# Performance work log

Measured on AMD Instinct MI355X. Metric: run time of the kernel, lower is better.

The kernel has to match this reference:

```python
import jax, jax.numpy as jnp
import numpy as np
import math

B, T, D, H = 4, 2048, 1024, 16
DK = D // H  # 64


def setup_inputs() -> dict:
    key = jax.random.key(0)
    ks = jax.random.split(key, 9)
    s = 0.02
    return {
        "x": jax.random.normal(ks[0], (B, T, D), jnp.float32),
        "wq": jax.random.normal(ks[1], (H, DK, D), jnp.float32) * s,
        "bq": jax.random.normal(ks[2], (H, DK), jnp.float32) * s,
        "wk": jax.random.normal(ks[3], (H, DK, D), jnp.float32) * s,
        "bk": jax.random.normal(ks[4], (H, DK), jnp.float32) * s,
        "wv": jax.random.normal(ks[5], (H, DK, D), jnp.float32) * s,
        "bv": jax.random.normal(ks[6], (H, DK), jnp.float32) * s,
        "wo": jax.random.normal(ks[7], (D, D), jnp.float32) * s,
        "bo": jax.random.normal(ks[8], (D,), jnp.float32) * s,
    }


def reference(x, wq, bq, wk, bk, wv, bv, wo, bo):
    # per-head projections (torch Linear: y = x @ W.T + b), all heads batched
    q = jnp.einsum("btc,hdc->bhtd", x, wq) + bq[None, :, None, :]
    k = jnp.einsum("btc,hdc->bhtd", x, wk) + bk[None, :, None, :]
    v = jnp.einsum("btc,hdc->bhtd", x, wv) + bv[None, :, None, :]
    scores = jnp.einsum("bhtd,bhsd->bhts", q, k) / math.sqrt(DK)
    causal = jnp.tril(jnp.ones((T, T), dtype=bool))  # True = keep
    scores = jnp.where(causal[None, None], scores, -jnp.inf)
    sm = jax.nn.softmax(scores, axis=-1)
    att = jnp.einsum("bhts,bhsd->bhtd", sm, v)
    # concat heads (head 0 first) -> [B, T, D]
    yh = att.transpose(0, 2, 1, 3).reshape(B, T, D)
    return yh @ wo.T + bo
```

## Files before the change

kernel.cpp:

```cpp
#include <hip/hip_runtime.h>
#include <hip/hip_bf16.h>
#include <cstdint>
#include <cstddef>

#define B_  4
#define T_  2048
#define D_  1024
#define H_  16
#define DK_ 64
#define M_  (B_ * T_)
#define NT8 (D_ / 64)

typedef __attribute__((ext_vector_type(8))) short bf16x8;
typedef __attribute__((ext_vector_type(4))) float f32x4;

static __device__ __forceinline__ unsigned short f2bf(float f) {
    __hip_bfloat16 h = __float2bfloat16(f);
    unsigned short u;
    __builtin_memcpy(&u, &h, 2);
    return u;
}

static __device__ __forceinline__ unsigned int pk2bf(float a, float b) {
    __hip_bfloat162 h = __float22bfloat162_rn(make_float2(a, b));
    unsigned int u;
    __builtin_memcpy(&u, &h, 4);
    return u;
}

static __device__ __forceinline__ void gl2lds16(const void* g, void* l) {
    __builtin_amdgcn_global_load_lds(
        (const __attribute__((address_space(1))) unsigned int*)g,
        (__attribute__((address_space(3))) unsigned int*)l,
        16, 0, 0);
}

__global__ __launch_bounds__(256) void cvt_bf16(
    const float* __restrict__ x,  const float* __restrict__ wq,
    const float* __restrict__ wk, const float* __restrict__ wv,
    const float* __restrict__ wo, unsigned short* __restrict__ dst)
{
    const int idx = blockIdx.x * 256 + threadIdx.x;
    const float* src;
    int off;
    if (idx < 2097152) { src = x; off = idx; }
    else {
        const int r = (idx - 2097152) >> 18;
        off = (idx - 2097152) & 262143;
        src = (r == 0) ? wq : (r == 1) ? wk : (r == 2) ? wv : wo;
    }
    float4 v = ((const float4*)src)[off];
    ushort4 o;
    o.x = f2bf(v.x); o.y = f2bf(v.y); o.z = f2bf(v.z); o.w = f2bf(v.w);
    ((ushort4*)dst)[idx] = o;
}

__global__ __launch_bounds__(512, 2) void gemm8p(
    const unsigned short* __restrict__ Amat,
    const unsigned short* __restrict__ w0,
    const unsigned short* __restrict__ w1,
    const unsigned short* __restrict__ w2,
    const float* __restrict__ b0,
    const float* __restrict__ b1,
    const float* __restrict__ b2,
    unsigned short* __restrict__ outU,
    float* __restrict__ outF,
    const int mode)
{
    const int s   = blockIdx.x;
    const int xcd = s & 7;
    const int idx = s >> 3;
    const int mm  = idx & 3;
    const int ns  = idx >> 2;
    const int sel = (mode == 0) ? (ns >> 3) : 3;
    const int nn  = (mode == 0) ? (ns & 7) : ns;
    const int m0  = (xcd * 4 + mm) * 256;
    const int n0  = nn * 128;

    const unsigned short* Bmat = (sel == 0) ? w0 : (sel == 1) ? w1 : w2;
    const float* bias          = (sel == 0) ? b0 : (sel == 1) ? b1 : b2;
    const bool selV = (sel == 2);

    const int tid  = threadIdx.x;
    const int w    = tid >> 6;
    const int lane = tid & 63;
    const int l15  = lane & 15, g = lane >> 4;
    const int lane8 = lane * 8;
    const int wm8  = (w >> 2) * 8;
    const int wn2  = (w & 3) * 2;

    __shared__ __align__(16) unsigned short As[2][32][512];
    __shared__ __align__(16) unsigned short Bs[2][16][512];

    f32x4 acc[8][2];
#pragma unroll
    for (int i = 0; i < 8; ++i)
#pragma unroll
        for (int j = 0; j < 2; ++j) acc[i][j] = (f32x4){0.f, 0.f, 0.f, 0.f};

    const unsigned short* aP[4];
#pragma unroll
    for (int j = 0; j < 4; ++j)
        aP[j] = Amat + (size_t)(m0 + (w >> 1) * 16 + 64 * j + l15) * D_
                     + (w & 1) * 32 + g * 8;
    const unsigned short* bP[2];
#pragma unroll
    for (int jb = 0; jb < 2; ++jb)
        bP[jb] = Bmat + (size_t)(n0 + w * 16 + l15) * D_ + jb * 32 + g * 8;

#pragma unroll
    for (int j = 0; j < 4; ++j) gl2lds16(aP[j], &As[0][w + 8 * j][0]);
    gl2lds16(bP[0], &Bs[0][2 * w    ][0]);
    gl2lds16(bP[1], &Bs[0][2 * w + 1][0]);
    gl2lds16(aP[0] + 64, &As[1][w     ][0]);
    gl2lds16(aP[2] + 64, &As[1][w + 16][0]);
    gl2lds16(bP[0] + 64, &Bs[1][2 * w    ][0]);
    gl2lds16(bP[1] + 64, &Bs[1][2 * w + 1][0]);
    asm volatile("s_waitcnt vmcnt(4)" ::: "memory");
    __builtin_amdgcn_s_barrier();

    bf16x8 bfr[2][2];
    bf16x8 ap[4][2];

    for (int kt = 0; kt < NT8; ++kt) {
        const int cur = kt & 1;
        const int ko  = kt * 64;

#pragma unroll
        for (int nj = 0; nj < 2; ++nj)
#pragma unroll
            for (int ks = 0; ks < 2; ++ks)
                bfr[nj][ks] = *(const bf16x8*)&Bs[cur][(wn2 + nj) * 2 + ks][lane8];
#pragma unroll
        for (int mi = 0; mi < 4; ++mi)
#pragma unroll
            for (int ks = 0; ks < 2; ++ks)
                ap[mi][ks] = *(const bf16x8*)&As[cur][(wm8 + mi) * 2 + ks][lane8];
        if (kt + 1 < NT8) {
            gl2lds16(aP[1] + ko + 64, &As[cur ^ 1][w + 8 ][0]);
            gl2lds16(aP[3] + ko + 64, &As[cur ^ 1][w + 24][0]);
        }
        __builtin_amdgcn_s_barrier();
        asm volatile("s_waitcnt lgkmcnt(0)" ::: "memory");
        __builtin_amdgcn_s_setprio(1);
        if (!selV) {
#pragma unroll
            for (int mi = 0; mi < 4; ++mi)
#pragma unroll
                for (int nj = 0; nj < 2; ++nj) {
                    acc[mi][nj] = __builtin_amdgcn_mfma_f32_16x16x32_bf16(
                        bfr[nj][0], ap[mi][0], acc[mi][nj], 0, 0, 0);
                    acc[mi][nj] = __builtin_amdgcn_mfma_f32_16x16x32_bf16(
                        bfr[nj][1], ap[mi][1], acc[mi][nj], 0, 0, 0);
                }
        } else {
#pragma unroll
            for (int mi = 0; mi < 4; ++mi)
#pragma unroll
                for (int nj = 0; nj < 2; ++nj) {
                    acc[mi][nj] = __builtin_amdgcn_mfma_f32_16x16x32_bf16(
                        ap[mi][0], bfr[nj][0], acc[mi][nj], 0, 0, 0);
                    acc[mi][nj] = __builtin_amdgcn_mfma_f32_16x16x32_bf16(
                        ap[mi][1], bfr[nj][1], acc[mi][nj], 0, 0, 0);
                }
        }
        __builtin_amdgcn_s_setprio(0);
        __builtin_amdgcn_s_barrier();

#pragma unroll
        for (int mi = 0; mi < 4; ++mi)
#pragma unroll
            for (int ks = 0; ks < 2; ++ks)
                ap[mi][ks] = *(const bf16x8*)&As[cur][(wm8 + 4 + mi) * 2 + ks][lane8];
        if (kt + 2 < NT8) {
            gl2lds16(aP[0] + ko + 128, &As[cur][w     ][0]);
            gl2lds16(aP[2] + ko + 128, &As[cur][w + 16][0]);
            gl2lds16(bP[0] + ko + 128, &Bs[cur][2 * w    ][0]);
            gl2lds16(bP[1] + ko + 128, &Bs[cur][2 * w + 1][0]);
        }
        __builtin_amdgcn_s_barrier();
        asm volatile("s_waitcnt lgkmcnt(0)" ::: "memory");
        __builtin_amdgcn_s_setprio(1);
        if (!selV) {
#pragma unroll
            for (int mi = 0; mi < 4; ++mi)
#pragma unroll
                for (int nj = 0; nj < 2; ++nj) {
                    acc[4 + mi][nj] = __builtin_amdgcn_mfma_f32_16x16x32_bf16(
                        bfr[nj][0], ap[mi][0], acc[4 + mi][nj], 0, 0, 0);
                    acc[4 + mi][nj] = __builtin_amdgcn_mfma_f32_16x16x32_bf16(
                        bfr[nj][1], ap[mi][1], acc[4 + mi][nj], 0, 0, 0);
                }
        } else {
#pragma unroll
            for (int mi = 0; mi < 4; ++mi)
#pragma unroll
                for (int nj = 0; nj < 2; ++nj) {
                    acc[4 + mi][nj] = __builtin_amdgcn_mfma_f32_16x16x32_bf16(
                        ap[mi][0], bfr[nj][0], acc[4 + mi][nj], 0, 0, 0);
                    acc[4 + mi][nj] = __builtin_amdgcn_mfma_f32_16x16x32_bf16(
                        ap[mi][1], bfr[nj][1], acc[4 + mi][nj], 0, 0, 0);
                }
        }
        __builtin_amdgcn_s_setprio(0);
        if (kt < NT8 - 2)       asm volatile("s_waitcnt vmcnt(4)" ::: "memory");
        else if (kt == NT8 - 2) asm volatile("s_waitcnt vmcnt(0)" ::: "memory");
        __builtin_amdgcn_s_barrier();
    }

    const int mbase = m0 + (w >> 2) * 128;
    const int nbase = n0 + (w & 3) * 32;
    const size_t BTD = (size_t)B_ * T_ * D_;

    if (mode == 1) {
#pragma unroll
        for (int nj = 0; nj < 2; ++nj) {
            const int ch0 = nbase + nj * 16 + g * 4;
            const float4 bb = *(const float4*)(bias + ch0);
#pragma unroll
            for (int mi = 0; mi < 8; ++mi) {
                const int tok = mbase + mi * 16 + l15;
                float4 r;
                r.x = acc[mi][nj][0] + bb.x;
                r.y = acc[mi][nj][1] + bb.y;
                r.z = acc[mi][nj][2] + bb.z;
                r.w = acc[mi][nj][3] + bb.w;
                *(float4*)(outF + (size_t)tok * D_ + ch0) = r;
            }
        }
    } else if (!selV) {
        unsigned short* outp = outU + (size_t)sel * BTD;
        const float osc = (sel == 0) ? 0.125f * 1.44269504f : 1.0f;
#pragma unroll
        for (int nj = 0; nj < 2; ++nj) {
            const int ch0 = nbase + nj * 16 + g * 4;
            const int hh = ch0 >> 6, dk0 = ch0 & 63;
            const float4 bb = *(const float4*)(bias + ch0);
#pragma unroll
            for (int mi = 0; mi < 8; ++mi) {
                const int tok = mbase + mi * 16 + l15;
                const int b = tok >> 11, t = tok & (T_ - 1);
                ushort4 r;
                r.x = f2bf((acc[mi][nj][0] + bb.x) * osc);
                r.y = f2bf((acc[mi][nj][1] + bb.y) * osc);
                r.z = f2bf((acc[mi][nj][2] + bb.z) * osc);
                r.w = f2bf((acc[mi][nj][3] + bb.w) * osc);
                *(ushort4*)(outp + ((size_t)((b * H_ + hh) * T_ + t)) * DK_ + dk0) = r;
            }
        }
    } else {
        unsigned short* outp = outU + 2 * BTD;
#pragma unroll
        for (int nj = 0; nj < 2; ++nj) {
            const int ch = nbase + nj * 16 + l15;
            const int hh = ch >> 6, dk = ch & 63;
            const float bbv = bias[ch];
#pragma unroll
            for (int mi = 0; mi < 8; ++mi) {
                const int tok0 = mbase + mi * 16 + g * 4;
                const int b = tok0 >> 11, t0 = tok0 & (T_ - 1);
                ushort4 r;
                r.x = f2bf(acc[mi][nj][0] + bbv);
                r.y = f2bf(acc[mi][nj][1] + bbv);
                r.z = f2bf(acc[mi][nj][2] + bbv);
                r.w = f2bf(acc[mi][nj][3] + bbv);
                *(ushort4*)(outp + ((size_t)((b * H_ + hh) * DK_ + dk)) * T_ + t0) = r;
            }
        }
    }
}

__global__ __launch_bounds__(256) void attn(
    const unsigned short* __restrict__ qg, const unsigned short* __restrict__ kg,
    const unsigned short* __restrict__ vtg,
    float* __restrict__ pO, float* __restrict__ pL,
    unsigned short* __restrict__ yh)
{
    const int s    = blockIdx.x;
    const int xcd  = s & 7;
    const int t_   = s >> 3;
    const int bhl  = t_ / 48;
    const int j    = t_ % 48;
    const int bh   = xcd * 8 + bhl;
    const int ridx = 47 - j;

    int x, ks;
    if (ridx < 16) { x = ridx; ks = 0; }
    else { const int r = ridx - 16; x = 16 + (r >> 1); ks = r & 1; }
    const int h   = bh & (H_ - 1);
    const int b   = bh >> 4;
    const int tq0 = x * 64;
    const int sBeg = ks << 10;
    const int sEnd = min(sBeg + 1024, tq0 + 64);
    const int nCh  = (sEnd - sBeg) >> 6;

    const int tid  = threadIdx.x;
    const int w    = tid >> 6;
    const int lane = tid & 63;
    const int l15  = lane & 15;
    const int g    = lane >> 4;

    const size_t base = (size_t)bh * T_ * DK_;
    const unsigned short* Qb  = qg  + base;
    const unsigned short* Kb  = kg  + base;
    const unsigned short* Vtb = vtg + base;

    __shared__ __align__(16) unsigned short Kf[8][512];
    __shared__ __align__(16) unsigned short Vf[8][512];
    __shared__ __align__(16) unsigned short Pb[4][16][68];

    const int q0w = tq0 + w * 16;
    const int tq  = q0w + l15;

    bf16x8 qf0 = *(const bf16x8*)(Qb + (size_t)tq * DK_ + g * 8);
    bf16x8 qf1 = *(const bf16x8*)(Qb + (size_t)tq * DK_ + 32 + g * 8);

    bf16x8 ones;
#pragma unroll
    for (int jj = 0; jj < 8; ++jj) ones[jj] = (short)0x3F80;

    f32x4 o[4];
#pragma unroll
    for (int i = 0; i < 4; ++i) o[i] = (f32x4){0.f, 0.f, 0.f, 0.f};
    f32x4 lacc = {0.f, 0.f, 0.f, 0.f};

    const unsigned short* kSrc = Kb + (size_t)(sBeg + w * 16 + l15) * DK_ + g * 8;
    const unsigned short* vSrc = Vtb + (size_t)(w * 16 + l15) * T_ + sBeg + g * 8;

    bf16x8 kr0 = *(const bf16x8*)(kSrc);
    bf16x8 kr1 = *(const bf16x8*)(kSrc + 32);
    bf16x8 vr0 = *(const bf16x8*)(vSrc);
    bf16x8 vr1 = *(const bf16x8*)(vSrc + 32);

    for (int ch = 0; ch < nCh; ++ch) {
        const int s0 = sBeg + ch * 64;
        __syncthreads();
        *(bf16x8*)&Kf[2 * w    ][lane * 8] = kr0;
        *(bf16x8*)&Kf[2 * w + 1][lane * 8] = kr1;
        *(bf16x8*)&Vf[2 * w    ][lane * 8] = vr0;
        *(bf16x8*)&Vf[2 * w + 1][lane * 8] = vr1;
        if (ch + 1 < nCh) {
            const size_t ko = (size_t)(ch + 1) * 64 * DK_;
            const int    vo = (ch + 1) * 64;
            kr0 = *(const bf16x8*)(kSrc + ko);
            kr1 = *(const bf16x8*)(kSrc + ko + 32);
            vr0 = *(const bf16x8*)(vSrc + vo);
            vr1 = *(const bf16x8*)(vSrc + vo + 32);
        }
        __syncthreads();

#pragma unroll
        for (int st = 0; st < 4; ++st) {
            const int sbase = s0 + st * 16;
            const bool live = (sbase <= q0w + 15);
            unsigned int pkl, pkh;
            if (live) {
                bf16x8 a0 = *(const bf16x8*)&Kf[st * 2 + 0][lane * 8];
                bf16x8 a1 = *(const bf16x8*)&Kf[st * 2 + 1][lane * 8];
                f32x4 sacc = {0.f, 0.f, 0.f, 0.f};
                sacc = __builtin_amdgcn_mfma_f32_16x16x32_bf16(a0, qf0, sacc, 0, 0, 0);
                sacc = __builtin_amdgcn_mfma_f32_16x16x32_bf16(a1, qf1, sacc, 0, 0, 0);
                float p0, p1, p2, p3;
                if (sbase + 15 > q0w) {
                    p0 = (sbase + g * 4 + 0 <= tq) ? exp2f(sacc[0]) : 0.f;
                    p1 = (sbase + g * 4 + 1 <= tq) ? exp2f(sacc[1]) : 0.f;
                    p2 = (sbase + g * 4 + 2 <= tq) ? exp2f(sacc[2]) : 0.f;
                    p3 = (sbase + g * 4 + 3 <= tq) ? exp2f(sacc[3]) : 0.f;
                } else {
                    p0 = exp2f(sacc[0]); p1 = exp2f(sacc[1]);
                    p2 = exp2f(sacc[2]); p3 = exp2f(sacc[3]);
                }
                pkl = pk2bf(p0, p1);
                pkh = pk2bf(p2, p3);
            } else {
                pkl = 0; pkh = 0;
            }
            uint2 pk; pk.x = pkl; pk.y = pkh;
            *(uint2*)&Pb[w][l15][st * 16 + g * 4] = pk;
        }

        bf16x8 pf0 = *(const bf16x8*)&Pb[w][l15][g * 8];
        bf16x8 pf1 = *(const bf16x8*)&Pb[w][l15][32 + g * 8];
        lacc = __builtin_amdgcn_mfma_f32_16x16x32_bf16(ones, pf0, lacc, 0, 0, 0);
        lacc = __builtin_amdgcn_mfma_f32_16x16x32_bf16(ones, pf1, lacc, 0, 0, 0);
#pragma unroll
        for (int dt = 0; dt < 4; ++dt) {
            bf16x8 v0 = *(const bf16x8*)&Vf[dt * 2 + 0][lane * 8];
            bf16x8 v1 = *(const bf16x8*)&Vf[dt * 2 + 1][lane * 8];
            o[dt] = __builtin_amdgcn_mfma_f32_16x16x32_bf16(v0, pf0, o[dt], 0, 0, 0);
            o[dt] = __builtin_amdgcn_mfma_f32_16x16x32_bf16(v1, pf1, o[dt], 0, 0, 0);
        }
    }

    if (tq0 < 1024) {
        const float inv = 1.f / lacc[0];
        unsigned short* yrow = yh + ((size_t)(b * T_ + tq)) * D_ + h * DK_;
#pragma unroll
        for (int dt = 0; dt < 4; ++dt) {
            ushort4 r;
            r.x = f2bf(o[dt][0] * inv); r.y = f2bf(o[dt][1] * inv);
            r.z = f2bf(o[dt][2] * inv); r.w = f2bf(o[dt][3] * inv);
            *(ushort4*)(yrow + dt * 16 + g * 4) = r;
        }
    } else {
        float* po = pO + ((size_t)ks * (B_ * H_) + bh) * (size_t)T_ * DK_
                       + (size_t)tq * DK_;
#pragma unroll
        for (int dt = 0; dt < 4; ++dt) {
            float4 r;
            r.x = o[dt][0]; r.y = o[dt][1]; r.z = o[dt][2]; r.w = o[dt][3];
            *(float4*)(po + dt * 16 + g * 4) = r;
        }
        if (g == 0)
            pL[((size_t)ks * (B_ * H_) + bh) * T_ + tq] = lacc[0];
    }
}

__global__ __launch_bounds__(256) void attn_reduce(
    const float* __restrict__ pO, const float* __restrict__ pL,
    unsigned short* __restrict__ yh)
{
    const int idx  = blockIdx.x * 256 + threadIdx.x;
    const int flat = idx * 4;
    const int dk = flat & 63;
    const int t  = 1024 + ((flat >> 6) & 1023);
    const int bh = flat >> 16;
    const int h = bh & (H_ - 1), b = bh >> 4;

    const size_t e0 = ((size_t)bh * T_ + t) * DK_ + dk;
    const size_t soff = (size_t)(B_ * H_) * T_ * DK_;
    float4 o  = *(const float4*)(pO + e0);
    float4 o1 = *(const float4*)(pO + soff + e0);
    o.x += o1.x; o.y += o1.y; o.z += o1.z; o.w += o1.w;
    const float l = pL[(size_t)bh * T_ + t]
                  + pL[(size_t)(B_ * H_) * T_ + (size_t)bh * T_ + t];
    const float inv = 1.f / l;
    ushort4 r;
    r.x = f2bf(o.x * inv); r.y = f2bf(o.y * inv);
    r.z = f2bf(o.z * inv); r.w = f2bf(o.w * inv);
    *(ushort4*)(yh + ((size_t)(b * T_ + t)) * D_ + h * DK_ + dk) = r;
}

extern "C" void kernel_launch(void* const* d_in, const int* in_sizes, int n_in,
                              void* d_out, int out_size, void* d_ws, size_t ws_size,
                              hipStream_t stream) {
    const float* x  = (const float*)d_in[0];
    const float* wq = (const float*)d_in[1];
    const float* bq = (const float*)d_in[2];
    const float* wk = (const float*)d_in[3];
    const float* bk = (const float*)d_in[4];
    const float* wv = (const float*)d_in[5];
    const float* bv = (const float*)d_in[6];
    const float* wo = (const float*)d_in[7];
    const float* bo = (const float*)d_in[8];
    float* out = (float*)d_out;

    const size_t BTD = (size_t)B_ * T_ * D_;
    const size_t WSZ = (size_t)D_ * D_;
    unsigned short* xb  = (unsigned short*)d_ws;
    unsigned short* wqb = xb  + BTD;
    unsigned short* wkb = wqb + WSZ;
    unsigned short* wvb = wkb + WSZ;
    unsigned short* wob = wvb + WSZ;
    unsigned short* qb  = wob + WSZ;
    unsigned short* kb  = qb  + BTD;
    unsigned short* vtb = kb  + BTD;
    unsigned short* yhb = vtb + BTD;
    float* pO = (float*)(yhb + BTD);
    float* pL = pO + 2 * BTD;

    cvt_bf16<<<dim3(12288), 256, 0, stream>>>(x, wq, wk, wv, wo, xb);

    gemm8p<<<dim3(768), 512, 0, stream>>>(
        xb, wqb, wkb, wvb, bq, bk, bv, qb, (float*)nullptr, 0);

    attn<<<dim3(3072), 256, 0, stream>>>(qb, kb, vtb, pO, pL, yhb);

    attn_reduce<<<dim3(4096), 256, 0, stream>>>(pO, pL, yhb);

    gemm8p<<<dim3(256), 512, 0, stream>>>(
        yhb, wob, wob, wob, bo, bo, bo, (unsigned short*)nullptr, out, 1);
}
```

Before: 328.7 us.

## Double attention query tile to 128 rows per block, two 16-row groups per wave

Each attention block now processes 128 query rows instead of 64, with each wave handling two 16-row query sub-tiles that share the same K/V fragments loaded from shared memory. This halves the block count and the K/V global and LDS loads per query row, and wave chunks entirely above the causal diagonal are now skipped. The cost is more registers per thread (two accumulator sets), larger P staging in shared memory, and fewer blocks, which may reduce occupancy and load balance.

```diff
diff --git a/kernel.cpp b/kernel.cpp
--- a/kernel.cpp
+++ b/kernel.cpp
@@ -279,19 +279,19 @@
     const int s    = blockIdx.x;
     const int xcd  = s & 7;
     const int t_   = s >> 3;
-    const int bhl  = t_ / 48;
-    const int j    = t_ % 48;
+    const int bhl  = t_ / 24;
+    const int j    = t_ % 24;
     const int bh   = xcd * 8 + bhl;
-    const int ridx = 47 - j;
+    const int ridx = 23 - j;
 
     int x, ks;
-    if (ridx < 16) { x = ridx; ks = 0; }
-    else { const int r = ridx - 16; x = 16 + (r >> 1); ks = r & 1; }
+    if (ridx < 8) { x = ridx; ks = 0; }
+    else { const int r = ridx - 8; x = 8 + (r >> 1); ks = r & 1; }
     const int h   = bh & (H_ - 1);
     const int b   = bh >> 4;
-    const int tq0 = x * 64;
+    const int tq0 = x * 128;
     const int sBeg = ks << 10;
-    const int sEnd = min(sBeg + 1024, tq0 + 64);
+    const int sEnd = min(sBeg + 1024, tq0 + 128);
     const int nCh  = (sEnd - sBeg) >> 6;
 
     const int tid  = threadIdx.x;
@@ -307,22 +307,29 @@
 
     __shared__ __align__(16) unsigned short Kf[8][512];
     __shared__ __align__(16) unsigned short Vf[8][512];
-    __shared__ __align__(16) unsigned short Pb[4][16][68];
-
-    const int q0w = tq0 + w * 16;
-    const int tq  = q0w + l15;
-
-    bf16x8 qf0 = *(const bf16x8*)(Qb + (size_t)tq * DK_ + g * 8);
-    bf16x8 qf1 = *(const bf16x8*)(Qb + (size_t)tq * DK_ + 32 + g * 8);
+    __shared__ __align__(16) unsigned short Pb[4][32][68];
+
+    const int q0w = tq0 + w * 32;
+    const int tqa = q0w + l15;
+    const int tqb = q0w + 16 + l15;
+
+    bf16x8 qfa0 = *(const bf16x8*)(Qb + (size_t)tqa * DK_ + g * 8);
+    bf16x8 qfa1 = *(const bf16x8*)(Qb + (size_t)tqa * DK_ + 32 + g * 8);
+    bf16x8 qfb0 = *(const bf16x8*)(Qb + (size_t)tqb * DK_ + g * 8);
+    bf16x8 qfb1 = *(const bf16x8*)(Qb + (size_t)tqb * DK_ + 32 + g * 8);
 
     bf16x8 ones;
 #pragma unroll
     for (int jj = 0; jj < 8; ++jj) ones[jj] = (short)0x3F80;
 
-    f32x4 o[4];
-#pragma unroll
-    for (int i = 0; i < 4; ++i) o[i] = (f32x4){0.f, 0.f, 0.f, 0.f};
-    f32x4 lacc = {0.f, 0.f, 0.f, 0.f};
+    f32x4 oa[4], ob[4];
+#pragma unroll
+    for (int i = 0; i < 4; ++i) {
+        oa[i] = (f32x4){0.f, 0.f, 0.f, 0.f};
+        ob[i] = (f32x4){0.f, 0.f, 0.f, 0.f};
+    }
+    f32x4 lacca = {0.f, 0.f, 0.f, 0.f};
+    f32x4 laccb = {0.f, 0.f, 0.f, 0.f};
 
     const unsigned short* kSrc = Kb + (size_t)(sBeg + w * 16 + l15) * DK_ + g * 8;
     const unsigned short* vSrc = Vtb + (size_t)(w * 16 + l15) * T_ + sBeg + g * 8;
@@ -349,70 +356,104 @@
         }
         __syncthreads();
 
+        if (s0 > q0w + 31) continue;
+
 #pragma unroll
         for (int st = 0; st < 4; ++st) {
             const int sbase = s0 + st * 16;
-            const bool live = (sbase <= q0w + 15);
-            unsigned int pkl, pkh;
-            if (live) {
-                bf16x8 a0 = *(const bf16x8*)&Kf[st * 2 + 0][lane * 8];
-                bf16x8 a1 = *(const bf16x8*)&Kf[st * 2 + 1][lane * 8];
+            bf16x8 a0 = *(const bf16x8*)&Kf[st * 2 + 0][lane * 8];
+            bf16x8 a1 = *(const bf16x8*)&Kf[st * 2 + 1][lane * 8];
+            uint2 pka; pka.x = 0u; pka.y = 0u;
+            uint2 pkb; pkb.x = 0u; pkb.y = 0u;
+            if (sbase <= q0w + 15) {
                 f32x4 sacc = {0.f, 0.f, 0.f, 0.f};
-                sacc = __builtin_amdgcn_mfma_f32_16x16x32_bf16(a0, qf0, sacc, 0, 0, 0);
-                sacc = __builtin_amdgcn_mfma_f32_16x16x32_bf16(a1, qf1, sacc, 0, 0, 0);
+                sacc = __builtin_amdgcn_mfma_f32_16x16x32_bf16(a0, qfa0, sacc, 0, 0, 0);
+                sacc = __builtin_amdgcn_mfma_f32_16x16x32_bf16(a1, qfa1, sacc, 0, 0, 0);
                 float p0, p1, p2, p3;
                 if (sbase + 15 > q0w) {
-                    p0 = (sbase + g * 4 + 0 <= tq) ? exp2f(sacc[0]) : 0.f;
-                    p1 = (sbase + g * 4 + 1 <= tq) ? exp2f(sacc[1]) : 0.f;
-                    p2 = (sbase + g * 4 + 2 <= tq) ? exp2f(sacc[2]) : 0.f;
-                    p3 = (sbase + g * 4 + 3 <= tq) ? exp2f(sacc[3]) : 0.f;
+                    p0 = (sbase + g * 4 + 0 <= tqa) ? exp2f(sacc[0]) : 0.f;
+                    p1 = (sbase + g * 4 + 1 <= tqa) ? exp2f(sacc[1]) : 0.f;
+                    p2 = (sbase + g * 4 + 2 <= tqa) ? exp2f(sacc[2]) : 0.f;
+                    p3 = (sbase + g * 4 + 3 <= tqa) ? exp2f(sacc[3]) : 0.f;
                 } else {
                     p0 = exp2f(sacc[0]); p1 = exp2f(sacc[1]);
                     p2 = exp2f(sacc[2]); p3 = exp2f(sacc[3]);
                 }
-                pkl = pk2bf(p0, p1);
-                pkh = pk2bf(p2, p3);
-            } else {
-                pkl = 0; pkh = 0;
+                pka.x = pk2bf(p0, p1);
+                pka.y = pk2bf(p2, p3);
             }
-            uint2 pk; pk.x = pkl; pk.y = pkh;
-            *(uint2*)&Pb[w][l15][st * 16 + g * 4] = pk;
-        }
-
-        bf16x8 pf0 = *(const bf16x8*)&Pb[w][l15][g * 8];
-        bf16x8 pf1 = *(const bf16x8*)&Pb[w][l15][32 + g * 8];
-        lacc = __builtin_amdgcn_mfma_f32_16x16x32_bf16(ones, pf0, lacc, 0, 0, 0);
-        lacc = __builtin_amdgcn_mfma_f32_16x16x32_bf16(ones, pf1, lacc, 0, 0, 0);
+            {
+                f32x4 sacc = {0.f, 0.f, 0.f, 0.f};
+                sacc = __builtin_amdgcn_mfma_f32_16x16x32_bf16(a0, qfb0, sacc, 0, 0, 0);
+                sacc = __builtin_amdgcn_mfma_f32_16x16x32_bf16(a1, qfb1, sacc, 0, 0, 0);
+                float p0, p1, p2, p3;
+                if (sbase + 15 > q0w + 16) {
+                    p0 = (sbase + g * 4 + 0 <= tqb) ? exp2f(sacc[0]) : 0.f;
+                    p1 = (sbase + g * 4 + 1 <= tqb) ? exp2f(sacc[1]) : 0.f;
+                    p2 = (sbase + g * 4 + 2 <= tqb) ? exp2f(sacc[2]) : 0.f;
+                    p3 = (sbase + g * 4 + 3 <= tqb) ? exp2f(sacc[3]) : 0.f;
+                } else {
+                    p0 = exp2f(sacc[0]); p1 = exp2f(sacc[1]);
+                    p2 = exp2f(sacc[2]); p3 = exp2f(sacc[3]);
+                }
+                pkb.x = pk2bf(p0, p1);
+                pkb.y = pk2bf(p2, p3);
+            }
+            *(uint2*)&Pb[w][l15     ][st * 16 + g * 4] = pka;
+            *(uint2*)&Pb[w][16 + l15][st * 16 + g * 4] = pkb;
+        }
+
+        bf16x8 pa0 = *(const bf16x8*)&Pb[w][l15     ][g * 8];
+        bf16x8 pa1 = *(const bf16x8*)&Pb[w][l15     ][32 + g * 8];
+        bf16x8 pb0 = *(const bf16x8*)&Pb[w][16 + l15][g * 8];
+        bf16x8 pb1 = *(const bf16x8*)&Pb[w][16 + l15][32 + g * 8];
+        lacca = __builtin_amdgcn_mfma_f32_16x16x32_bf16(ones, pa0, lacca, 0, 0, 0);
+        lacca = __builtin_amdgcn_mfma_f32_16x16x32_bf16(ones, pa1, lacca, 0, 0, 0);
+        laccb = __builtin_amdgcn_mfma_f32_16x16x32_bf16(ones, pb0, laccb, 0, 0, 0);
+        laccb = __builtin_amdgcn_mfma_f32_16x16x32_bf16(ones, pb1, laccb, 0, 0, 0);
 #pragma unroll
         for (int dt = 0; dt < 4; ++dt) {
             bf16x8 v0 = *(const bf16x8*)&Vf[dt * 2 + 0][lane * 8];
             bf16x8 v1 = *(const bf16x8*)&Vf[dt * 2 + 1][lane * 8];
-            o[dt] = __builtin_amdgcn_mfma_f32_16x16x32_bf16(v0, pf0, o[dt], 0, 0, 0);
-            o[dt] = __builtin_amdgcn_mfma_f32_16x16x32_bf16(v1, pf1, o[dt], 0, 0, 0);
+            oa[dt] = __builtin_amdgcn_mfma_f32_16x16x32_bf16(v0, pa0, oa[dt], 0, 0, 0);
+            oa[dt] = __builtin_amdgcn_mfma_f32_16x16x32_bf16(v1, pa1, oa[dt], 0, 0, 0);
+            ob[dt] = __builtin_amdgcn_mfma_f32_16x16x32_bf16(v0, pb0, ob[dt], 0, 0, 0);
+            ob[dt] = __builtin_amdgcn_mfma_f32_16x16x32_bf16(v1, pb1, ob[dt], 0, 0, 0);
         }
     }
 
     if (tq0 < 1024) {
-        const float inv = 1.f / lacc[0];
-        unsigned short* yrow = yh + ((size_t)(b * T_ + tq)) * D_ + h * DK_;
+        const float inva = 1.f / lacca[0];
+        const float invb = 1.f / laccb[0];
+        unsigned short* ya = yh + ((size_t)(b * T_ + tqa)) * D_ + h * DK_;
+        unsigned short* yb = yh + ((size_t)(b * T_ + tqb)) * D_ + h * DK_;
 #pragma unroll
         for (int dt = 0; dt < 4; ++dt) {
-            ushort4 r;
-            r.x = f2bf(o[dt][0] * inv); r.y = f2bf(o[dt][1] * inv);
-            r.z = f2bf(o[dt][2] * inv); r.w = f2bf(o[dt][3] * inv);
-            *(ushort4*)(yrow + dt * 16 + g * 4) = r;
+            ushort4 ra, rb;
+            ra.x = f2bf(oa[dt][0] * inva); ra.y = f2bf(oa[dt][1] * inva);
+            ra.z = f2bf(oa[dt][2] * inva); ra.w = f2bf(oa[dt][3] * inva);
+            rb.x = f2bf(ob[dt][0] * invb); rb.y = f2bf(ob[dt][1] * invb);
+            rb.z = f2bf(ob[dt][2] * invb); rb.w = f2bf(ob[dt][3] * invb);
+            *(ushort4*)(ya + dt * 16 + g * 4) = ra;
+            *(ushort4*)(yb + dt * 16 + g * 4) = rb;
         }
     } else {
-        float* po = pO + ((size_t)ks * (B_ * H_) + bh) * (size_t)T_ * DK_
-                       + (size_t)tq * DK_;
+        float* poa = pO + ((size_t)ks * (B_ * H_) + bh) * (size_t)T_ * DK_
+                        + (size_t)tqa * DK_;
+        float* pob = pO + ((size_t)ks * (B_ * H_) + bh) * (size_t)T_ * DK_
+                        + (size_t)tqb * DK_;
 #pragma unroll
         for (int dt = 0; dt < 4; ++dt) {
-            float4 r;
-            r.x = o[dt][0]; r.y = o[dt][1]; r.z = o[dt][2]; r.w = o[dt][3];
-            *(float4*)(po + dt * 16 + g * 4) = r;
-        }
-        if (g == 0)
-            pL[((size_t)ks * (B_ * H_) + bh) * T_ + tq] = lacc[0];
+            float4 ra, rb;
+            ra.x = oa[dt][0]; ra.y = oa[dt][1]; ra.z = oa[dt][2]; ra.w = oa[dt][3];
+            rb.x = ob[dt][0]; rb.y = ob[dt][1]; rb.z = ob[dt][2]; rb.w = ob[dt][3];
+            *(float4*)(poa + dt * 16 + g * 4) = ra;
+            *(float4*)(pob + dt * 16 + g * 4) = rb;
+        }
+        if (g == 0) {
+            pL[((size_t)ks * (B_ * H_) + bh) * T_ + tqa] = lacca[0];
+            pL[((size_t)ks * (B_ * H_) + bh) * T_ + tqb] = laccb[0];
+        }
     }
 }
 
@@ -474,7 +515,7 @@
     gemm8p<<<dim3(768), 512, 0, stream>>>(
         xb, wqb, wkb, wvb, bq, bk, bv, qb, (float*)nullptr, 0);
 
-    attn<<<dim3(3072), 256, 0, stream>>>(qb, kb, vtb, pO, pL, yhb);
+    attn<<<dim3(1536), 256, 0, stream>>>(qb, kb, vtb, pO, pL, yhb);
 
     attn_reduce<<<dim3(4096), 256, 0, stream>>>(pO, pL, yhb);
 
```

New measurement: 338.7 us. +3.0%, slower.

## Drop split-KV attention and reduce kernel; raise MFMA wave priority

Applied to the files above, without the earlier changes.

Removes the key-range split for the later query tiles, so each block now handles one full causal query tile, longest first. This drops the fp32 partial-output writes, the partial sums and the separate attn_reduce launch. The cost is fewer blocks (2048 instead of 3072) and a longer tail from the longest tiles, which now take up to 32 chunks. It also wraps the MFMA section in s_setprio so that waves issuing matrix ops get scheduling priority.

```diff
diff --git a/kernel.cpp b/kernel.cpp
--- a/kernel.cpp
+++ b/kernel.cpp
@@ -273,26 +273,19 @@
 __global__ __launch_bounds__(256) void attn(
     const unsigned short* __restrict__ qg, const unsigned short* __restrict__ kg,
     const unsigned short* __restrict__ vtg,
-    float* __restrict__ pO, float* __restrict__ pL,
     unsigned short* __restrict__ yh)
 {
     const int s    = blockIdx.x;
     const int xcd  = s & 7;
     const int t_   = s >> 3;
-    const int bhl  = t_ / 48;
-    const int j    = t_ % 48;
+    const int bhl  = t_ >> 5;
+    const int j    = t_ & 31;
     const int bh   = xcd * 8 + bhl;
-    const int ridx = 47 - j;
-
-    int x, ks;
-    if (ridx < 16) { x = ridx; ks = 0; }
-    else { const int r = ridx - 16; x = 16 + (r >> 1); ks = r & 1; }
-    const int h   = bh & (H_ - 1);
-    const int b   = bh >> 4;
-    const int tq0 = x * 64;
-    const int sBeg = ks << 10;
-    const int sEnd = min(sBeg + 1024, tq0 + 64);
-    const int nCh  = (sEnd - sBeg) >> 6;
+    const int x    = 31 - j;
+    const int h    = bh & (H_ - 1);
+    const int b    = bh >> 4;
+    const int tq0  = x * 64;
+    const int nCh  = x + 1;
 
     const int tid  = threadIdx.x;
     const int w    = tid >> 6;
@@ -324,8 +317,8 @@
     for (int i = 0; i < 4; ++i) o[i] = (f32x4){0.f, 0.f, 0.f, 0.f};
     f32x4 lacc = {0.f, 0.f, 0.f, 0.f};
 
-    const unsigned short* kSrc = Kb + (size_t)(sBeg + w * 16 + l15) * DK_ + g * 8;
-    const unsigned short* vSrc = Vtb + (size_t)(w * 16 + l15) * T_ + sBeg + g * 8;
+    const unsigned short* kSrc = Kb + (size_t)(w * 16 + l15) * DK_ + g * 8;
+    const unsigned short* vSrc = Vtb + (size_t)(w * 16 + l15) * T_ + g * 8;
 
     bf16x8 kr0 = *(const bf16x8*)(kSrc);
     bf16x8 kr1 = *(const bf16x8*)(kSrc + 32);
@@ -333,7 +326,7 @@
     bf16x8 vr1 = *(const bf16x8*)(vSrc + 32);
 
     for (int ch = 0; ch < nCh; ++ch) {
-        const int s0 = sBeg + ch * 64;
+        const int s0 = ch * 64;
         __syncthreads();
         *(bf16x8*)&Kf[2 * w    ][lane * 8] = kr0;
         *(bf16x8*)&Kf[2 * w + 1][lane * 8] = kr1;
@@ -381,6 +374,7 @@
 
         bf16x8 pf0 = *(const bf16x8*)&Pb[w][l15][g * 8];
         bf16x8 pf1 = *(const bf16x8*)&Pb[w][l15][32 + g * 8];
+        __builtin_amdgcn_s_setprio(1);
         lacc = __builtin_amdgcn_mfma_f32_16x16x32_bf16(ones, pf0, lacc, 0, 0, 0);
         lacc = __builtin_amdgcn_mfma_f32_16x16x32_bf16(ones, pf1, lacc, 0, 0, 0);
 #pragma unroll
@@ -390,55 +384,18 @@
             o[dt] = __builtin_amdgcn_mfma_f32_16x16x32_bf16(v0, pf0, o[dt], 0, 0, 0);
             o[dt] = __builtin_amdgcn_mfma_f32_16x16x32_bf16(v1, pf1, o[dt], 0, 0, 0);
         }
+        __builtin_amdgcn_s_setprio(0);
     }
 
-    if (tq0 < 1024) {
-        const float inv = 1.f / lacc[0];
-        unsigned short* yrow = yh + ((size_t)(b * T_ + tq)) * D_ + h * DK_;
-#pragma unroll
-        for (int dt = 0; dt < 4; ++dt) {
-            ushort4 r;
-            r.x = f2bf(o[dt][0] * inv); r.y = f2bf(o[dt][1] * inv);
-            r.z = f2bf(o[dt][2] * inv); r.w = f2bf(o[dt][3] * inv);
-            *(ushort4*)(yrow + dt * 16 + g * 4) = r;
-        }
-    } else {
-        float* po = pO + ((size_t)ks * (B_ * H_) + bh) * (size_t)T_ * DK_
-                       + (size_t)tq * DK_;
-#pragma unroll
-        for (int dt = 0; dt < 4; ++dt) {
-            float4 r;
-            r.x = o[dt][0]; r.y = o[dt][1]; r.z = o[dt][2]; r.w = o[dt][3];
-            *(float4*)(po + dt * 16 + g * 4) = r;
-        }
-        if (g == 0)
-            pL[((size_t)ks * (B_ * H_) + bh) * T_ + tq] = lacc[0];
+    const float inv = 1.f / lacc[0];
+    unsigned short* yrow = yh + ((size_t)(b * T_ + tq)) * D_ + h * DK_;
+#pragma unroll
+    for (int dt = 0; dt < 4; ++dt) {
+        ushort4 r;
+        r.x = f2bf(o[dt][0] * inv); r.y = f2bf(o[dt][1] * inv);
+        r.z = f2bf(o[dt][2] * inv); r.w = f2bf(o[dt][3] * inv);
+        *(ushort4*)(yrow + dt * 16 + g * 4) = r;
     }
-}
-
-__global__ __launch_bounds__(256) void attn_reduce(
-    const float* __restrict__ pO, const float* __restrict__ pL,
-    unsigned short* __restrict__ yh)
-{
-    const int idx  = blockIdx.x * 256 + threadIdx.x;
-    const int flat = idx * 4;
-    const int dk = flat & 63;
-    const int t  = 1024 + ((flat >> 6) & 1023);
-    const int bh = flat >> 16;
-    const int h = bh & (H_ - 1), b = bh >> 4;
-
-    const size_t e0 = ((size_t)bh * T_ + t) * DK_ + dk;
-    const size_t soff = (size_t)(B_ * H_) * T_ * DK_;
-    float4 o  = *(const float4*)(pO + e0);
-    float4 o1 = *(const float4*)(pO + soff + e0);
-    o.x += o1.x; o.y += o1.y; o.z += o1.z; o.w += o1.w;
-    const float l = pL[(size_t)bh * T_ + t]
-                  + pL[(size_t)(B_ * H_) * T_ + (size_t)bh * T_ + t];
-    const float inv = 1.f / l;
-    ushort4 r;
-    r.x = f2bf(o.x * inv); r.y = f2bf(o.y * inv);
-    r.z = f2bf(o.z * inv); r.w = f2bf(o.w * inv);
-    *(ushort4*)(yh + ((size_t)(b * T_ + t)) * D_ + h * DK_ + dk) = r;
 }
 
 extern "C" void kernel_launch(void* const* d_in, const int* in_sizes, int n_in,
@@ -466,17 +423,13 @@
     unsigned short* kb  = qb  + BTD;
     unsigned short* vtb = kb  + BTD;
     unsigned short* yhb = vtb + BTD;
-    float* pO = (float*)(yhb + BTD);
-    float* pL = pO + 2 * BTD;
 
     cvt_bf16<<<dim3(12288), 256, 0, stream>>>(x, wq, wk, wv, wo, xb);
 
     gemm8p<<<dim3(768), 512, 0, stream>>>(
         xb, wqb, wkb, wvb, bq, bk, bv, qb, (float*)nullptr, 0);
 
-    attn<<<dim3(3072), 256, 0, stream>>>(qb, kb, vtb, pO, pL, yhb);
-
-    attn_reduce<<<dim3(4096), 256, 0, stream>>>(pO, pL, yhb);
+    attn<<<dim3(2048), 256, 0, stream>>>(qb, kb, vtb, yhb);
 
     gemm8p<<<dim3(256), 512, 0, stream>>>(
         yhb, wob, wob, wob, bo, bo, bo, (unsigned short*)nullptr, out, 1);
```

After: 319.2 us (median of 2 runs). 1.03x faster.
